# Kernel tuning notes

Hardware: AMD Instinct MI355X
Metric: run time of the kernel (lower is better)

The kernel has to match this reference:

```python
import jax, jax.numpy as jnp
import numpy as np

T = 262144   # total tokens across the ragged batch
D = 256      # dim_token
B = 2048     # number of sequences


def setup_inputs() -> dict:
    key = jax.random.key(0)
    k1, k2, k3 = jax.random.split(key, 3)
    x_flat = jax.random.normal(k1, (T, D), dtype=jnp.float32)
    seg_ids = jnp.sort(jax.random.randint(k2, (T,), 0, B)).astype(jnp.int64)
    # kaiming_uniform-ish init for the class token weight
    bound = 1.0 / np.sqrt(D)
    weight = jax.random.uniform(k3, (1, D), dtype=jnp.float32, minval=-bound, maxval=bound)
    return {"x_flat": x_flat, "weight": weight, "seg_ids": seg_ids, "num_segments": B}


def reference(x_flat, weight, seg_ids, num_segments):
    # Packed ragged class-token prepend.
    # Input:  x_flat [T, D] packed rows, seg_ids [T] sorted sequence ids in [0, B).
    # Output: [T + B, D] packed rows where each sequence s gains one leading
    # class-token row (equivalent to torch.cat([weight, seq]) per sequence).
    Ttot, Dd = x_flat.shape
    # offsets[s] = start of sequence s in the input packed layout
    offsets = jnp.searchsorted(seg_ids, jnp.arange(num_segments))
    # In the output layout, sequence s starts at offsets[s] + s (each prior
    # sequence gained one row), so its class token lands at offsets[s] + s
    class_idx = offsets + jnp.arange(num_segments)
    # token at input flat index i (seq s, pos p) moves to i + s + 1
    tok_idx = jnp.arange(Ttot) + seg_ids + 1
    out = jnp.zeros((Ttot + num_segments, Dd), dtype=x_flat.dtype)
    out = out.at[class_idx].set(jnp.broadcast_to(weight, (num_segments, Dd)))
    out = out.at[tok_idx].set(x_flat)
    return out
```

## Files before the change

### kernel.cpp

```cpp
#include <hip/hip_runtime.h>


constexpr int DTOK = 256;
constexpr int V4   = DTOK / 4;

__global__ __launch_bounds__(256) void ctn_copy_tokens(
    const float4* __restrict__ x,
    const int* __restrict__ seg,
    float4* __restrict__ out,
    long long total_vec)
{
    long long stride = (long long)gridDim.x * blockDim.x;
    for (long long idx = (long long)blockIdx.x * blockDim.x + threadIdx.x;
         idx < total_vec; idx += stride) {
        int row = (int)(idx >> 6);
        int col = (int)(idx & (V4 - 1));
        int s   = seg[row];
        float4 v = x[idx];
        long long orow = (long long)row + s + 1;
        out[orow * V4 + col] = v;
    }
}

__global__ __launch_bounds__(256) void ctn_class_tokens(
    const float4* __restrict__ w,
    const int* __restrict__ seg,
    float4* __restrict__ out,
    int T, int B)
{
    int gid  = blockIdx.x * blockDim.x + threadIdx.x;
    int s    = gid >> 6;
    int lane = gid & 63;
    if (s >= B) return;
    int lo = 0, hi = T;
    while (lo < hi) {
        int mid = (lo + hi) >> 1;
        if (seg[mid] < s) lo = mid + 1; else hi = mid;
    }
    long long orow = (long long)lo + s;
    out[orow * V4 + lane] = w[lane];
}

extern "C" void kernel_launch(void* const* d_in, const int* in_sizes, int n_in,
                              void* d_out, int out_size, void* d_ws, size_t ws_size,
                              hipStream_t stream) {
    const float* x_flat = (const float*)d_in[0];
    const float* weight = (const float*)d_in[1];
    const int*   seg    = (const int*)d_in[2];
    int T = in_sizes[2];
    int B = out_size / DTOK - T;

    float* out = (float*)d_out;

    long long total_vec = (long long)T * V4;
    int blkA = 2048;
    ctn_copy_tokens<<<blkA, 256, 0, stream>>>(
        (const float4*)x_flat, seg, (float4*)out, total_vec);

    int blkB = (B * 64 + 255) / 256;
    ctn_class_tokens<<<blkB, 256, 0, stream>>>(
        (const float4*)weight, seg, (float4*)out, T, B);
}
```

Baseline: 450.2 us.

## Fuse token copy and class-token writes into one wave-per-row kernel

Merges the two kernels into a single launch in which each wavefront copies one token row and writes the class-token rows for any segments that begin at that row, found by comparing seg[row-1] and seg[row]. This removes the per-segment binary search over seg and the second launch. Loads and stores now use nontemporal builtins to stream past the cache. Row offsets are computed in 32-bit int, which stays in range for these sizes, and trailing empty segments are handled by the last row.

```diff
diff --git a/kernel.cpp b/kernel.cpp
--- a/kernel.cpp
+++ b/kernel.cpp
@@ -4,41 +4,35 @@
 constexpr int DTOK = 256;
 constexpr int V4   = DTOK / 4;
 
-__global__ __launch_bounds__(256) void ctn_copy_tokens(
-    const float4* __restrict__ x,
+typedef float f4 __attribute__((ext_vector_type(4)));
+
+__global__ __launch_bounds__(256) void ctn_fused(
+    const f4* __restrict__ x,
     const int* __restrict__ seg,
-    float4* __restrict__ out,
-    long long total_vec)
-{
-    long long stride = (long long)gridDim.x * blockDim.x;
-    for (long long idx = (long long)blockIdx.x * blockDim.x + threadIdx.x;
-         idx < total_vec; idx += stride) {
-        int row = (int)(idx >> 6);
-        int col = (int)(idx & (V4 - 1));
-        int s   = seg[row];
-        float4 v = x[idx];
-        long long orow = (long long)row + s + 1;
-        out[orow * V4 + col] = v;
-    }
-}
-
-__global__ __launch_bounds__(256) void ctn_class_tokens(
-    const float4* __restrict__ w,
-    const int* __restrict__ seg,
-    float4* __restrict__ out,
+    const f4* __restrict__ w,
+    f4*       __restrict__ out,
     int T, int B)
 {
-    int gid  = blockIdx.x * blockDim.x + threadIdx.x;
-    int s    = gid >> 6;
-    int lane = gid & 63;
-    if (s >= B) return;
-    int lo = 0, hi = T;
-    while (lo < hi) {
-        int mid = (lo + hi) >> 1;
-        if (seg[mid] < s) lo = mid + 1; else hi = mid;
+    const int lane = threadIdx.x & 63;
+    const int wid  = (blockIdx.x * blockDim.x + threadIdx.x) >> 6;
+    const int nw   = (gridDim.x * blockDim.x) >> 6;
+
+    const f4 wv = w[lane];
+
+    for (int row = wid; row < T; row += nw) {
+        const int s = seg[row];
+        const f4 v = __builtin_nontemporal_load(&x[row * V4 + lane]);
+        __builtin_nontemporal_store(v, &out[(row + s + 1) * V4 + lane]);
+
+        const int sp = (row == 0) ? -1 : seg[row - 1];
+        for (int t = sp + 1; t <= s; ++t)
+            __builtin_nontemporal_store(wv, &out[(row + t) * V4 + lane]);
+
+        if (row == T - 1) {
+            for (int t = s + 1; t < B; ++t)
+                __builtin_nontemporal_store(wv, &out[(T + t) * V4 + lane]);
+        }
     }
-    long long orow = (long long)lo + s;
-    out[orow * V4 + lane] = w[lane];
 }
 
 extern "C" void kernel_launch(void* const* d_in, const int* in_sizes, int n_in,
@@ -47,17 +41,10 @@
     const float* x_flat = (const float*)d_in[0];
     const float* weight = (const float*)d_in[1];
     const int*   seg    = (const int*)d_in[2];
-    int T = in_sizes[2];
-    int B = out_size / DTOK - T;
+    const int T = in_sizes[2];
+    const int B = out_size / DTOK - T;
 
-    float* out = (float*)d_out;
-
-    long long total_vec = (long long)T * V4;
-    int blkA = 2048;
-    ctn_copy_tokens<<<blkA, 256, 0, stream>>>(
-        (const float4*)x_flat, seg, (float4*)out, total_vec);
-
-    int blkB = (B * 64 + 255) / 256;
-    ctn_class_tokens<<<blkB, 256, 0, stream>>>(
-        (const float4*)weight, seg, (float4*)out, T, B);
+    ctn_fused<<<2048, 256, 0, stream>>>(
+        (const f4*)x_flat, seg, (const f4*)weight,
+        (f4*)d_out, T, B);
 }
```

New measurement: 425.6 us. -5.5%, faster.
